# Kernel tuning notes

Measured on AMD Instinct MI355X. Metric: run time of the kernel, lower is better.

The kernel has to match this reference:

```python
import jax, jax.numpy as jnp
import numpy as np

B, S, D_IN = 64, 3072, 128
E, H, OUT = 64, 256, 10
K, STRIDE = 3, 3
T_OUT = (S - K) // STRIDE + 1  # 1024


def setup_inputs() -> dict:
    key = jax.random.key(0)
    ks = jax.random.split(key, 8)
    inputs = jax.random.normal(ks[0], (B, S, D_IN), dtype=jnp.float32)
    r = jnp.zeros((B, E, T_OUT), dtype=jnp.float32)
    s = 0.05
    conv_w = jax.random.normal(ks[1], (E, D_IN, K), dtype=jnp.float32) * s
    conv_b = jax.random.normal(ks[2], (E,), dtype=jnp.float32) * s
    w_ih = jax.random.normal(ks[3], (4 * H, E), dtype=jnp.float32) * s
    w_hh = jax.random.normal(ks[4], (4 * H, H), dtype=jnp.float32) * s
    b_ih = jax.random.normal(ks[5], (4 * H,), dtype=jnp.float32) * s
    b_hh = jax.random.normal(ks[6], (4 * H,), dtype=jnp.float32) * s
    lin_w = jax.random.normal(ks[7], (OUT, H), dtype=jnp.float32) * s
    lin_b = jnp.zeros((OUT,), dtype=jnp.float32)
    return {"inputs": inputs, "r": r, "batch_size": B,
            "conv_w": conv_w, "conv_b": conv_b,
            "w_ih": w_ih, "w_hh": w_hh, "b_ih": b_ih, "b_hh": b_hh,
            "lin_w": lin_w, "lin_b": lin_b}


def _forward(inputs, conv_w, conv_b, w_ih, w_hh, b_ih, b_hh, lin_w, lin_b):
    # F.normalize(inputs, dim=2): L2-normalize feature dim (eps=1e-12)
    norm = jnp.linalg.norm(inputs, axis=2, keepdims=True)
    x = inputs / jnp.maximum(norm, 1e-12)
    # permute(0,2,1): [B, D_IN, S], then Conv1d stride 3
    x = jnp.transpose(x, (0, 2, 1))
    emb = jax.lax.conv_general_dilated(
        x, conv_w, window_strides=(STRIDE,), padding='VALID',
        dimension_numbers=('NCH', 'OIH', 'NCH'))
    emb = emb + conv_b[None, :, None]
    act = jax.nn.relu(emb)                      # [B, E, T_OUT]
    xs = jnp.transpose(act, (2, 0, 1))          # [T, B, E] for scan

    def step(carry, x_t):
        h, c = carry
        gates = x_t @ w_ih.T + b_ih + h @ w_hh.T + b_hh  # [B, 4H]
        i_g, f_g, g_g, o_g = jnp.split(gates, 4, axis=1)
        c_new = jax.nn.sigmoid(f_g) * c + jax.nn.sigmoid(i_g) * jnp.tanh(g_g)
        h_new = jax.nn.sigmoid(o_g) * jnp.tanh(c_new)
        return (h_new, c_new), None

    h0 = jnp.zeros((inputs.shape[0], H), dtype=inputs.dtype)
    c0 = jnp.zeros((inputs.shape[0], H), dtype=inputs.dtype)
    (h_last, _), _ = jax.lax.scan(step, (h0, c0), xs)
    return h_last @ lin_w.T + lin_b             # [B, OUT]


def reference(inputs, r, batch_size, conv_w, conv_b, w_ih, w_hh, b_ih, b_hh, lin_w, lin_b):
    # mode='plain': r and batch_size are unused by the math
    return _forward(inputs, conv_w, conv_b, w_ih, w_hh, b_ih, b_hh, lin_w, lin_b)
```

## Files before the change

### kernel.cpp

```cpp
#include <hip/hip_runtime.h>
#include <math.h>

#define B_   64
#define S_   3072
#define DIN  128
#define E_   64
#define H_   256
#define OUT_ 10
#define T_   1024
#define NG   32
#define GB   2
#define NCH  8
#define ROWS 128
#define GBH  (GB*H_)

#define SLOTS_PER_CHUNK 22
#define SLOTS_TOTAL     (NCH*SLOTS_PER_CHUNK)
#define HB_PAR_FLOATS   (SLOTS_TOTAL*4)
#define HB_GRP_FLOATS   (2*HB_PAR_FLOATS)

#define ACT_BYTES   (B_*E_*T_*4)
#define HBUF_OFF    ACT_BYTES
#define HBUF_BYTES  (NG*HB_GRP_FLOATS*4)
#define HFINAL_OFF  (HBUF_OFF + 184320)
#define HFINAL_BYTES (NG*GBH*4)

typedef float f32x4 __attribute__((ext_vector_type(4)));

__device__ __forceinline__ f32x4 coh_load_f32x4(const float* p) {
  f32x4 r;
  asm volatile("global_load_dwordx4 %0, %1, off sc0 sc1\n\ts_waitcnt vmcnt(0)"
               : "=v"(r) : "v"(p) : "memory");
  return r;
}
__device__ __forceinline__ void coh_store_f32x4(float* p, f32x4 v) {
  asm volatile("global_store_dwordx4 %0, %1, off sc0 sc1" :: "v"(p), "v"(v) : "memory");
}

__device__ __forceinline__ float fast_sigmoid(float x) {
  return __builtin_amdgcn_rcpf(1.0f + __expf(-x));
}
__device__ __forceinline__ float fast_tanh(float x) {
  return 2.0f * __builtin_amdgcn_rcpf(1.0f + __expf(-2.0f * x)) - 1.0f;
}

__global__ __launch_bounds__(512, 1) void conv_kernel(
    const float* __restrict__ in,
    const float* __restrict__ cw,
    const float* __restrict__ cb,
    float* __restrict__ actT)
{
  extern __shared__ float xs[];
  float4* xs4 = (float4*)xs;
  const int bid = blockIdx.x;
  const int b  = bid >> 4;
  const int tb = bid & 15;
  const int tid = threadIdx.x;

  const float4* gin = (const float4*)(in + (size_t)b*S_*DIN + (size_t)tb*192*DIN);
  #pragma unroll
  for (int i = 0; i < 12; ++i) {
    int f4 = tid + i*512;
    int r = f4 >> 5, dq = f4 & 31;
    xs4[r*32 + (dq ^ (r & 7))] = gin[f4];
  }
  __syncthreads();

  const int wv = tid >> 6, ln = tid & 63;
  for (int rr = 0; rr < 24; ++rr) {
    int r = wv*24 + rr;
    int u = r*32 + ((ln >> 1) ^ (r & 7));
    float2* p = (float2*)((char*)xs + (size_t)u*16 + (size_t)(ln & 1)*8);
    float2 v = *p;
    float s = v.x*v.x + v.y*v.y;
    #pragma unroll
    for (int off = 32; off >= 1; off >>= 1) s += __shfl_xor(s, off);
    float inv = 1.0f / fmaxf(sqrtf(s), 1e-12f);
    v.x *= inv; v.y *= inv;
    *p = v;
  }
  __syncthreads();

  const int eo = __builtin_amdgcn_readfirstlane(wv);
  float acc[8];
  #pragma unroll
  for (int j = 0; j < 8; ++j) acc[j] = cb[eo*8 + j];

  const int r0 = 3*ln, r1 = 3*ln + 1, r2 = 3*ln + 2;
  #pragma unroll 4
  for (int dq = 0; dq < 32; ++dq) {
    float4 x0 = xs4[r0*32 + (dq ^ (r0 & 7))];
    float4 x1 = xs4[r1*32 + (dq ^ (r1 & 7))];
    float4 x2 = xs4[r2*32 + (dq ^ (r2 & 7))];
    #pragma unroll
    for (int j = 0; j < 8; ++j) {
      const float* wp = cw + (size_t)(eo*8 + j)*(DIN*3) + dq*12;
      acc[j] += x0.x*wp[0] + x1.x*wp[1] + x2.x*wp[2]
              + x0.y*wp[3] + x1.y*wp[4] + x2.y*wp[5]
              + x0.z*wp[6] + x1.z*wp[7] + x2.z*wp[8]
              + x0.w*wp[9] + x1.w*wp[10] + x2.w*wp[11];
    }
  }

  const int tg = tb*64 + ln;
  #pragma unroll
  for (int j = 0; j < 8; ++j) {
    int e = eo*8 + j;
    actT[(size_t)b*E_*T_ + (size_t)e*T_ + tg] = fmaxf(acc[j], 0.0f);
  }
}

__global__ __launch_bounds__(256, 1) void lstm_kernel(
    const float* __restrict__ actT,
    const float* __restrict__ w_ih,
    const float* __restrict__ w_hh,
    const float* __restrict__ b_ih,
    const float* __restrict__ b_hh,
    float* hbuf,
    float* hfinal)
{
  __shared__ float h_lds[GBH];
  __shared__ float x_lds[GB*E_];
  __shared__ float scratch[4][ROWS][GB];
  __shared__ float bias_lds[ROWS];

  const int bid = blockIdx.x;
  const int g = bid & 31;
  const int q = bid >> 5;
  const int tid = threadIdx.x;
  const int lane = tid & 63;
  const int kq = tid >> 6;

  const int ra = lane, rb = lane + 64;
  const int growa = (ra >> 5)*256 + 32*q + (ra & 31);
  const int growb = (rb >> 5)*256 + 32*q + (rb & 31);

  float4 wr0[16], wr1[16], wi0[4], wi1[4];
  {
    const float4* pa = (const float4*)(w_hh + (size_t)growa*H_ + kq*64);
    const float4* pb = (const float4*)(w_hh + (size_t)growb*H_ + kq*64);
    #pragma unroll
    for (int i = 0; i < 16; ++i) { wr0[i] = pa[i]; wr1[i] = pb[i]; }
    const float4* qa = (const float4*)(w_ih + (size_t)growa*E_ + kq*16);
    const float4* qb = (const float4*)(w_ih + (size_t)growb*E_ + kq*16);
    #pragma unroll
    for (int i = 0; i < 4; ++i) { wi0[i] = qa[i]; wi1[i] = qb[i]; }
  }
  if (kq == 0) {
    bias_lds[ra] = b_ih[growa] + b_hh[growa];
    bias_lds[rb] = b_ih[growb] + b_hh[growb];
  }
  ((float2*)h_lds)[tid] = make_float2(0.0f, 0.0f);

  float* hgrp = hbuf + (size_t)g*HB_GRP_FLOATS;
  const int xb = (tid >> 6) & 1, xe = lane;
  const float* actp = actT + (size_t)(g*GB + xb)*E_*T_ + (size_t)xe*T_;
  const int uh = tid & 31, ub = (tid >> 5) & 1;

  const int sq = tid / SLOTS_PER_CHUNK;
  const int sj = tid % SLOTS_PER_CHUNK;
  const int sl = 3*sj;

  if (tid < 128) x_lds[xb*E_ + xe] = actp[0];
  __syncthreads();

  float c = 0.0f;
  for (int t = 0; t < T_; ++t) {
    float a0=0.f, a1=0.f, b0=0.f, b1=0.f;
    {
      const float* xp = x_lds + kq*16;
      #pragma unroll
      for (int i = 0; i < 4; ++i) {
        float4 w0 = wi0[i], w1 = wi1[i];
        float4 x0 = *(const float4*)(xp + 0*E_ + i*4);
        float4 x1 = *(const float4*)(xp + 1*E_ + i*4);
        a0 += w0.x*x0.x + w0.y*x0.y + w0.z*x0.z + w0.w*x0.w;
        a1 += w0.x*x1.x + w0.y*x1.y + w0.z*x1.z + w0.w*x1.w;
        b0 += w1.x*x0.x + w1.y*x0.y + w1.z*x0.z + w1.w*x0.w;
        b1 += w1.x*x1.x + w1.y*x1.y + w1.z*x1.z + w1.w*x1.w;
      }
    }
    float xpre = actp[(t + 1 < T_) ? (t + 1) : t];

    if (t > 0 && tid < SLOTS_TOTAL) {
      const float* sp = hgrp + (size_t)(t & 1)*HB_PAR_FLOATS + tid*4;
      f32x4 v;
      for (;;) {
        v = coh_load_f32x4(sp);
        if (__float_as_int(v[3]) == t) break;
      }
      h_lds[((sl    >> 5))*H_ + 32*sq + (sl     & 31)] = v[0];
      if (sl + 1 < 64) h_lds[(((sl+1) >> 5))*H_ + 32*sq + ((sl+1) & 31)] = v[1];
      if (sl + 2 < 64) h_lds[(((sl+2) >> 5))*H_ + 32*sq + ((sl+2) & 31)] = v[2];
    }
    __syncthreads();

    {
      const float* hp = h_lds + kq*64;
      #pragma unroll
      for (int i = 0; i < 16; ++i) {
        float4 w0 = wr0[i], w1 = wr1[i];
        float4 h0 = *(const float4*)(hp + 0*H_ + i*4);
        float4 h1 = *(const float4*)(hp + 1*H_ + i*4);
        a0 += w0.x*h0.x + w0.y*h0.y + w0.z*h0.z + w0.w*h0.w;
        a1 += w0.x*h1.x + w0.y*h1.y + w0.z*h1.z + w0.w*h1.w;
        b0 += w1.x*h0.x + w1.y*h0.y + w1.z*h0.z + w1.w*h0.w;
        b1 += w1.x*h1.x + w1.y*h1.y + w1.z*h1.z + w1.w*h1.w;
      }
    }
    *(float2*)&scratch[kq][ra][0] = make_float2(a0, a1);
    *(float2*)&scratch[kq][rb][0] = make_float2(b0, b1);
    __syncthreads();

    if (tid < 64) {
      float gi = bias_lds[uh],      gf = bias_lds[32+uh];
      float gg = bias_lds[64+uh],   go = bias_lds[96+uh];
      #pragma unroll
      for (int k = 0; k < 4; ++k) {
        gi += scratch[k][uh][ub];
        gf += scratch[k][32+uh][ub];
        gg += scratch[k][64+uh][ub];
        go += scratch[k][96+uh][ub];
      }
      float si = fast_sigmoid(gi);
      float sf = fast_sigmoid(gf);
      float so = fast_sigmoid(go);
      c = sf*c + si*fast_tanh(gg);
      float h = so*fast_tanh(c);

      int j = lane;
      int s1 = (3*j + 1 < 64) ? 3*j + 1 : 63;
      int s2 = (3*j + 2 < 64) ? 3*j + 2 : 63;
      float v0 = __shfl(h, 3*j, 64);
      float v1 = __shfl(h, s1, 64);
      float v2 = __shfl(h, s2, 64);
      if (j < SLOTS_PER_CHUNK) {
        f32x4 line;
        line[0] = v0; line[1] = v1; line[2] = v2;
        line[3] = __int_as_float(t + 1);
        float* dp = hgrp + (size_t)((t+1) & 1)*HB_PAR_FLOATS
                  + (size_t)(q*SLOTS_PER_CHUNK + j)*4;
        coh_store_f32x4(dp, line);
      }
      if (t == T_ - 1) {
        hfinal[(size_t)g*GBH + ub*H_ + 32*q + uh] = h;
      }
    }
    if (tid < 128) x_lds[xb*E_ + xe] = xpre;
    __syncthreads();
  }
}

__global__ void head_kernel(const float* __restrict__ hfinal,
                            const float* __restrict__ lw,
                            const float* __restrict__ lb,
                            float* __restrict__ out)
{
  int idx = blockIdx.x*blockDim.x + threadIdx.x;
  if (idx >= B_*OUT_) return;
  int b = idx / OUT_, o = idx % OUT_;
  int g = b >> 1, bl = b & 1;
  const float* h = hfinal + (size_t)g*GBH + (size_t)bl*H_;
  const float* w = lw + (size_t)o*H_;
  float s = lb[o];
  #pragma unroll 8
  for (int k = 0; k < H_; ++k) s += h[k]*w[k];
  out[idx] = s;
}

extern "C" void kernel_launch(void* const* d_in, const int* in_sizes, int n_in,
                              void* d_out, int out_size, void* d_ws, size_t ws_size,
                              hipStream_t stream) {
  const float* inputs = (const float*)d_in[0];
  const float* conv_w = (const float*)d_in[3];
  const float* conv_b = (const float*)d_in[4];
  const float* w_ih   = (const float*)d_in[5];
  const float* w_hh   = (const float*)d_in[6];
  const float* b_ih   = (const float*)d_in[7];
  const float* b_hh   = (const float*)d_in[8];
  const float* lin_w  = (const float*)d_in[9];
  const float* lin_b  = (const float*)d_in[10];

  float* actT   = (float*)d_ws;
  float* hbuf   = (float*)((char*)d_ws + HBUF_OFF);
  float* hfinal = (float*)((char*)d_ws + HFINAL_OFF);

  hipMemsetAsync(hbuf, 0, HBUF_BYTES, stream);
  hipLaunchKernelGGL(conv_kernel, dim3(B_*16), dim3(512), 192*128*4, stream,
                     inputs, conv_w, conv_b, actT);
  hipLaunchKernelGGL(lstm_kernel, dim3(NG*NCH), dim3(256), 0, stream,
                     actT, w_ih, w_hh, b_ih, b_hh, hbuf, hfinal);
  hipLaunchKernelGGL(head_kernel, dim3(3), dim3(256), 0, stream,
                     hfinal, lin_w, lin_b, (float*)d_out);
}
```

Before: 2.562 ms.

## Restructure LSTM step so each thread owns a full gate row

Each thread now keeps an entire gate row of w_hh and w_ih in registers and computes the full dot product itself. This removes the LDS scratch reduction across four waves and one of the two block barriers per timestep. The four gates of a hidden unit are gathered with xor shuffles, and the h exchange between blocks now uses one line per hidden unit that all 256 threads poll with a wave-wide check. Final h is read by the head kernel straight from the exchange buffer. In exchange, each thread runs a long serial FMA chain and holds about 320 VGPRs of weights, which risks spills or higher per-step latency.

```diff
diff --git a/kernel.cpp b/kernel.cpp
--- a/kernel.cpp
+++ b/kernel.cpp
@@ -11,19 +11,11 @@
 #define NG   32
 #define GB   2
 #define NCH  8
-#define ROWS 128
-#define GBH  (GB*H_)
-
-#define SLOTS_PER_CHUNK 22
-#define SLOTS_TOTAL     (NCH*SLOTS_PER_CHUNK)
-#define HB_PAR_FLOATS   (SLOTS_TOTAL*4)
-#define HB_GRP_FLOATS   (2*HB_PAR_FLOATS)
+#define GLINES 256
 
 #define ACT_BYTES   (B_*E_*T_*4)
 #define HBUF_OFF    ACT_BYTES
-#define HBUF_BYTES  (NG*HB_GRP_FLOATS*4)
-#define HFINAL_OFF  (HBUF_OFF + 184320)
-#define HFINAL_BYTES (NG*GBH*4)
+#define HBUF_BYTES  (NG*2*GLINES*16)
 
 typedef float f32x4 __attribute__((ext_vector_type(4)));
 
@@ -116,142 +108,95 @@
     const float* __restrict__ w_hh,
     const float* __restrict__ b_ih,
     const float* __restrict__ b_hh,
-    float* hbuf,
-    float* hfinal)
+    float* hbuf)
 {
-  __shared__ float h_lds[GBH];
-  __shared__ float x_lds[GB*E_];
-  __shared__ float scratch[4][ROWS][GB];
-  __shared__ float bias_lds[ROWS];
+  __shared__ float sl[2][2][320];
 
   const int bid = blockIdx.x;
   const int g = bid & 31;
   const int q = bid >> 5;
   const int tid = threadIdx.x;
-  const int lane = tid & 63;
-  const int kq = tid >> 6;
-
-  const int ra = lane, rb = lane + 64;
-  const int growa = (ra >> 5)*256 + 32*q + (ra & 31);
-  const int growb = (rb >> 5)*256 + 32*q + (rb & 31);
-
-  float4 wr0[16], wr1[16], wi0[4], wi1[4];
+  const int w = tid >> 6;
+  const int l = tid & 63;
+
+  const int hh = 8*w + (l >> 3);
+  const int b  = (l >> 2) & 1;
+  const int m  = l & 3;
+  const int row = m*256 + 32*q + hh;
+
+  const int hidx = tid;
+
+  const int xb = (tid >> 6) & 1, xe = tid & 63;
+
+  float4 wv[80];
   {
-    const float4* pa = (const float4*)(w_hh + (size_t)growa*H_ + kq*64);
-    const float4* pb = (const float4*)(w_hh + (size_t)growb*H_ + kq*64);
-    #pragma unroll
-    for (int i = 0; i < 16; ++i) { wr0[i] = pa[i]; wr1[i] = pb[i]; }
-    const float4* qa = (const float4*)(w_ih + (size_t)growa*E_ + kq*16);
-    const float4* qb = (const float4*)(w_ih + (size_t)growb*E_ + kq*16);
-    #pragma unroll
-    for (int i = 0; i < 4; ++i) { wi0[i] = qa[i]; wi1[i] = qb[i]; }
-  }
-  if (kq == 0) {
-    bias_lds[ra] = b_ih[growa] + b_hh[growa];
-    bias_lds[rb] = b_ih[growb] + b_hh[growb];
-  }
-  ((float2*)h_lds)[tid] = make_float2(0.0f, 0.0f);
-
-  float* hgrp = hbuf + (size_t)g*HB_GRP_FLOATS;
-  const int xb = (tid >> 6) & 1, xe = lane;
-  const float* actp = actT + (size_t)(g*GB + xb)*E_*T_ + (size_t)xe*T_;
-  const int uh = tid & 31, ub = (tid >> 5) & 1;
-
-  const int sq = tid / SLOTS_PER_CHUNK;
-  const int sj = tid % SLOTS_PER_CHUNK;
-  const int sl = 3*sj;
-
-  if (tid < 128) x_lds[xb*E_ + xe] = actp[0];
-  __syncthreads();
+    const float4* ph = (const float4*)(w_hh + (size_t)row*H_);
+    #pragma unroll
+    for (int i = 0; i < 64; ++i) wv[i] = ph[i];
+    const float4* px = (const float4*)(w_ih + (size_t)row*E_);
+    #pragma unroll
+    for (int i = 0; i < 16; ++i) wv[64+i] = px[i];
+  }
+  const float bias = b_ih[row] + b_hh[row];
+
+  sl[0][0][tid] = 0.f; sl[0][1][tid] = 0.f;
+  sl[1][0][tid] = 0.f; sl[1][1][tid] = 0.f;
+
+  float* hb = hbuf + (size_t)g * (2*GLINES*4);
+  const float* actp = actT + (size_t)((g*GB + xb)*E_ + xe) * T_;
 
   float c = 0.0f;
   for (int t = 0; t < T_; ++t) {
-    float a0=0.f, a1=0.f, b0=0.f, b1=0.f;
+    const int p = t & 1;
+    float xval = 0.f;
+    if (tid < 128) xval = actp[t];
+
+    if (t > 0) {
+      const float* lp = hb + (size_t)(p*GLINES + hidx)*4;
+      f32x4 v = coh_load_f32x4(lp);
+      while (!__all(__float_as_int(v[3]) == t)) v = coh_load_f32x4(lp);
+      sl[p][0][hidx] = v[0];
+      sl[p][1][hidx] = v[1];
+    }
+    if (tid < 128) sl[p][xb][256 + xe] = xval;
+    __syncthreads();
+
+    float acc = bias;
     {
-      const float* xp = x_lds + kq*16;
+      const float* hs = &sl[p][b][0];
       #pragma unroll
-      for (int i = 0; i < 4; ++i) {
-        float4 w0 = wi0[i], w1 = wi1[i];
-        float4 x0 = *(const float4*)(xp + 0*E_ + i*4);
-        float4 x1 = *(const float4*)(xp + 1*E_ + i*4);
-        a0 += w0.x*x0.x + w0.y*x0.y + w0.z*x0.z + w0.w*x0.w;
-        a1 += w0.x*x1.x + w0.y*x1.y + w0.z*x1.z + w0.w*x1.w;
-        b0 += w1.x*x0.x + w1.y*x0.y + w1.z*x0.z + w1.w*x0.w;
-        b1 += w1.x*x1.x + w1.y*x1.y + w1.z*x1.z + w1.w*x1.w;
+      for (int i = 0; i < 80; ++i) {
+        float4 hv = *(const float4*)(hs + i*4);
+        acc += wv[i].x*hv.x + wv[i].y*hv.y + wv[i].z*hv.z + wv[i].w*hv.w;
       }
     }
-    float xpre = actp[(t + 1 < T_) ? (t + 1) : t];
-
-    if (t > 0 && tid < SLOTS_TOTAL) {
-      const float* sp = hgrp + (size_t)(t & 1)*HB_PAR_FLOATS + tid*4;
-      f32x4 v;
-      for (;;) {
-        v = coh_load_f32x4(sp);
-        if (__float_as_int(v[3]) == t) break;
-      }
-      h_lds[((sl    >> 5))*H_ + 32*sq + (sl     & 31)] = v[0];
-      if (sl + 1 < 64) h_lds[(((sl+1) >> 5))*H_ + 32*sq + ((sl+1) & 31)] = v[1];
-      if (sl + 2 < 64) h_lds[(((sl+2) >> 5))*H_ + 32*sq + ((sl+2) & 31)] = v[2];
-    }
-    __syncthreads();
-
-    {
-      const float* hp = h_lds + kq*64;
-      #pragma unroll
-      for (int i = 0; i < 16; ++i) {
-        float4 w0 = wr0[i], w1 = wr1[i];
-        float4 h0 = *(const float4*)(hp + 0*H_ + i*4);
-        float4 h1 = *(const float4*)(hp + 1*H_ + i*4);
-        a0 += w0.x*h0.x + w0.y*h0.y + w0.z*h0.z + w0.w*h0.w;
-        a1 += w0.x*h1.x + w0.y*h1.y + w0.z*h1.z + w0.w*h1.w;
-        b0 += w1.x*h0.x + w1.y*h0.y + w1.z*h0.z + w1.w*h0.w;
-        b1 += w1.x*h1.x + w1.y*h1.y + w1.z*h1.z + w1.w*h1.w;
-      }
-    }
-    *(float2*)&scratch[kq][ra][0] = make_float2(a0, a1);
-    *(float2*)&scratch[kq][rb][0] = make_float2(b0, b1);
-    __syncthreads();
-
-    if (tid < 64) {
-      float gi = bias_lds[uh],      gf = bias_lds[32+uh];
-      float gg = bias_lds[64+uh],   go = bias_lds[96+uh];
-      #pragma unroll
-      for (int k = 0; k < 4; ++k) {
-        gi += scratch[k][uh][ub];
-        gf += scratch[k][32+uh][ub];
-        gg += scratch[k][64+uh][ub];
-        go += scratch[k][96+uh][ub];
-      }
-      float si = fast_sigmoid(gi);
-      float sf = fast_sigmoid(gf);
-      float so = fast_sigmoid(go);
-      c = sf*c + si*fast_tanh(gg);
-      float h = so*fast_tanh(c);
-
-      int j = lane;
-      int s1 = (3*j + 1 < 64) ? 3*j + 1 : 63;
-      int s2 = (3*j + 2 < 64) ? 3*j + 2 : 63;
-      float v0 = __shfl(h, 3*j, 64);
-      float v1 = __shfl(h, s1, 64);
-      float v2 = __shfl(h, s2, 64);
-      if (j < SLOTS_PER_CHUNK) {
-        f32x4 line;
-        line[0] = v0; line[1] = v1; line[2] = v2;
-        line[3] = __int_as_float(t + 1);
-        float* dp = hgrp + (size_t)((t+1) & 1)*HB_PAR_FLOATS
-                  + (size_t)(q*SLOTS_PER_CHUNK + j)*4;
-        coh_store_f32x4(dp, line);
-      }
-      if (t == T_ - 1) {
-        hfinal[(size_t)g*GBH + ub*H_ + 32*q + uh] = h;
-      }
-    }
-    if (tid < 128) x_lds[xb*E_ + xe] = xpre;
-    __syncthreads();
-  }
-}
-
-__global__ void head_kernel(const float* __restrict__ hfinal,
+
+    float x1 = __shfl_xor(acc, 1);
+    float x2 = __shfl_xor(acc, 2);
+    float x3 = __shfl_xor(x1, 2);
+    float gi = (m==0)?acc:(m==1)?x1:(m==2)?x2:x3;
+    float gf = (m==0)?x1 :(m==1)?acc:(m==2)?x3:x2;
+    float gg = (m==0)?x2 :(m==1)?x3 :(m==2)?acc:x1;
+    float go = (m==0)?x3 :(m==1)?x2 :(m==2)?x1 :acc;
+
+    float si = fast_sigmoid(gi);
+    float sf = fast_sigmoid(gf);
+    float so = fast_sigmoid(go);
+    c = sf*c + si*fast_tanh(gg);
+    float h = so*fast_tanh(c);
+
+    float h1 = __shfl(h, (l & 56) + 4, 64);
+    if ((l & 7) == 0) {
+      f32x4 line;
+      line[0] = h; line[1] = h1; line[2] = 0.f;
+      line[3] = __int_as_float(t + 1);
+      float* dp = hb + (size_t)((((t+1) & 1)*GLINES) + 32*q + hh)*4;
+      coh_store_f32x4(dp, line);
+    }
+  }
+}
+
+__global__ void head_kernel(const float* __restrict__ hbuf,
                             const float* __restrict__ lw,
                             const float* __restrict__ lb,
                             float* __restrict__ out)
@@ -260,11 +205,11 @@
   if (idx >= B_*OUT_) return;
   int b = idx / OUT_, o = idx % OUT_;
   int g = b >> 1, bl = b & 1;
-  const float* h = hfinal + (size_t)g*GBH + (size_t)bl*H_;
-  const float* w = lw + (size_t)o*H_;
+  const float* lines = hbuf + (size_t)g*(2*GLINES*4);
+  const float* wv = lw + (size_t)o*H_;
   float s = lb[o];
   #pragma unroll 8
-  for (int k = 0; k < H_; ++k) s += h[k]*w[k];
+  for (int k = 0; k < H_; ++k) s += lines[(size_t)k*4 + bl] * wv[k];
   out[idx] = s;
 }
 
@@ -281,15 +226,14 @@
   const float* lin_w  = (const float*)d_in[9];
   const float* lin_b  = (const float*)d_in[10];
 
-  float* actT   = (float*)d_ws;
-  float* hbuf   = (float*)((char*)d_ws + HBUF_OFF);
-  float* hfinal = (float*)((char*)d_ws + HFINAL_OFF);
+  float* actT = (float*)d_ws;
+  float* hbuf = (float*)((char*)d_ws + HBUF_OFF);
 
   hipMemsetAsync(hbuf, 0, HBUF_BYTES, stream);
   hipLaunchKernelGGL(conv_kernel, dim3(B_*16), dim3(512), 192*128*4, stream,
                      inputs, conv_w, conv_b, actT);
   hipLaunchKernelGGL(lstm_kernel, dim3(NG*NCH), dim3(256), 0, stream,
-                     actT, w_ih, w_hh, b_ih, b_hh, hbuf, hfinal);
+                     actT, w_ih, w_hh, b_ih, b_hh, hbuf);
   hipLaunchKernelGGL(head_kernel, dim3(3), dim3(256), 0, stream,
-                     hfinal, lin_w, lin_b, (float*)d_out);
-}
+                     hbuf, lin_w, lin_b, (float*)d_out);
+}
```

Result: slower. 4.182 ms (+63.3%).
